# Kernel tuning notes

Hardware: AMD Instinct MI355X
Metric: run time of the kernel (lower is better)

Reference implementation:

```python
import jax, jax.numpy as jnp
import numpy as np

B, E, S, H, HD, M, MLP = 8, 1024, 2000, 16, 64, 10, 4096
EPS = 1e-5

def setup_inputs() -> dict:
    key = jax.random.key(0)
    ks = jax.random.split(key, 12)
    s = lambda k, shape, sc: jax.random.normal(k, shape, dtype=jnp.float32) * sc
    return {
        'X': s(ks[0], (B, E, S), 1.0),
        'Wq': s(ks[1], (H, HD, E), E ** -0.5), 'bq': s(ks[2], (H, HD), 0.02),
        'Wk': s(ks[3], (H, HD, E), E ** -0.5), 'bk': s(ks[4], (H, HD), 0.02),
        'Wv': s(ks[5], (H, HD, E), E ** -0.5), 'bv': s(ks[6], (H, HD), 0.02),
        'g1': jnp.ones((E,), jnp.float32), 'be1': jnp.zeros((E,), jnp.float32),
        'W1': s(ks[7], (MLP, E), E ** -0.5), 'b1': s(ks[8], (MLP,), 0.02),
        'W2': s(ks[9], (E, MLP), MLP ** -0.5), 'b2': s(ks[10], (E,), 0.02),
        'g2': jnp.ones((E,), jnp.float32), 'be2': jnp.zeros((E,), jnp.float32),
    }

def iterative_inv(K, n_iter=6):
    I = jnp.eye(K.shape[-1], dtype=K.dtype)
    # global (over all batch/head) max row-sum * max col-sum init, as in Nystromformer
    V = K.swapaxes(-1, -2) / (jnp.max(jnp.sum(jnp.abs(K), axis=-2)) * jnp.max(jnp.sum(jnp.abs(K), axis=-1)))
    for _ in range(n_iter):
        KV = K @ V
        V = 0.25 * V @ (13.0 * I - KV @ (15.0 * I - KV @ (7.0 * I - KV)))
    return V

def layer_norm(x, g, b):
    mu = jnp.mean(x, axis=-1, keepdims=True)
    var = jnp.var(x, axis=-1, keepdims=True)
    return (x - mu) * jax.lax.rsqrt(var + EPS) * g + b

def reference(X, Wq, bq, Wk, bk, Wv, bv, g1, be1, W1, b1, W2, b2, g2, be2):
    x = jnp.swapaxes(X, 1, 2)  # (B, S, E)
    # per-head projections (stacked): (B, H, S, HD)
    Q = jnp.einsum('bse,hde->bhsd', x, Wq) + bq[None, :, None, :]
    K = jnp.einsum('bse,hde->bhsd', x, Wk) + bk[None, :, None, :]
    V = jnp.einsum('bse,hde->bhsd', x, Wv) + bv[None, :, None, :]
    scale = 1.0 / np.sqrt(np.sqrt(HD)).astype(np.float32)
    Q = Q * scale
    K = K * scale
    # landmarks: mean over segments of length S//M -> (B, H, M, HD)
    Ql = Q.reshape(B, H, M, S // M, HD).mean(axis=-2)
    Kl = K.reshape(B, H, M, S // M, HD).mean(axis=-2)
    k1 = jax.nn.softmax(jnp.einsum('bhsd,bhmd->bhsm', Q, Kl), axis=-1)   # (B,H,S,M)
    k2 = jax.nn.softmax(jnp.einsum('bhnd,bhmd->bhnm', Ql, Kl), axis=-1)  # (B,H,M,M)
    k3 = jax.nn.softmax(jnp.einsum('bhmd,bhsd->bhms', Ql, K), axis=-1)   # (B,H,M,S)
    attn = (k1 @ iterative_inv(k2)) @ (k3 @ V)  # (B,H,S,HD)
    attn = jnp.swapaxes(attn, 1, 2).reshape(B, S, E)
    h = layer_norm(attn, g1, be1)
    h = jax.nn.gelu(h @ W1.T + b1, approximate=False)
    h = h @ W2.T + b2
    h = layer_norm(h, g2, be2)
    return jnp.swapaxes(h, 2, 1)  # (B, E, S)
```

## Files before the change

### kernel.cpp

```cpp
#include <hip/hip_runtime.h>
#include <cmath>
#include <cstdint>
#include <cstddef>

#define BB 8
#define EE 1024
#define SS 2000
#define HH 16
#define HDIM 64
#define MLM 10
#define MLPD 4096
#define QKV_N 3072
#define MPAD 16384
#define QK_SCALE 0.35355339059327373f

typedef __attribute__((ext_vector_type(8))) short short8v;
typedef __attribute__((ext_vector_type(4))) float f32x4;

static __device__ __forceinline__ short f2bf(float x) {
  unsigned u = __builtin_bit_cast(unsigned, x);
  unsigned r = (u + 0x7fffu + ((u >> 16) & 1u)) >> 16;
  return (short)(unsigned short)r;
}
static __device__ __forceinline__ float bf2f(short x) {
  unsigned u = ((unsigned)(unsigned short)x) << 16;
  return __builtin_bit_cast(float, u);
}

static __device__ __forceinline__ void load_lds16(const short* g, short* l) {
  __builtin_amdgcn_global_load_lds(
      (const __attribute__((address_space(1))) void*)g,
      (__attribute__((address_space(3))) void*)l, 16, 0, 0);
}

__global__ __launch_bounds__(256) void transpose_x(const float* __restrict__ X, short* __restrict__ xb) {
  __shared__ float tile[32][33];
  int b = blockIdx.z;
  int e0 = blockIdx.y * 32;
  int s0 = blockIdx.x * 32;
  int tx = threadIdx.x;
  int ty = threadIdx.y;
#pragma unroll
  for (int i = 0; i < 32; i += 8) {
    int e = e0 + ty + i, s = s0 + tx;
    tile[ty + i][tx] = (s < SS) ? X[((size_t)b * EE + e) * SS + s] : 0.f;
  }
  __syncthreads();
#pragma unroll
  for (int i = 0; i < 32; i += 8) {
    int s = s0 + ty + i, e = e0 + tx;
    if (s < SS) xb[((size_t)b * SS + s) * EE + e] = f2bf(tile[tx][ty + i]);
  }
}

__global__ __launch_bounds__(256) void cast_f2b(const float* __restrict__ src, short* __restrict__ dst, int n) {
  int i = blockIdx.x * 256 + threadIdx.x;
  int stride = gridDim.x * 256;
  for (; i < n; i += stride) dst[i] = f2bf(src[i]);
}

__global__ __launch_bounds__(512, 2) void gemm256(
    const short* __restrict__ A, const short* __restrict__ Bm, void* __restrict__ Cv,
    int K, int N, int mode, int Mstore,
    const float* __restrict__ p0, const float* __restrict__ p1, const float* __restrict__ p2)
{
  __shared__ __align__(16) short lds[65536];
  const int tid = threadIdx.x;

  const int xcd = blockIdx.x & 7;
  const int idx = blockIdx.x >> 3;
  const int m0 = (((xcd << 3) | (idx & 7))) << 8;
  const int n0 = (idx >> 3) << 8;

  const int lane = tid & 63, wv = tid >> 6;
  const int wm = wv >> 2, wn = wv & 3;
  const int lm = lane & 15, quad = lane >> 4;
  const int swz = ((lm >> 3) & 1) << 1;
  const int aoff = (wm * 128 + lm) * 32 + ((quad ^ swz) << 3);
  const int boff = (wn * 64  + lm) * 32 + ((quad ^ swz) << 3);

  const int srow = tid >> 2;
  const int ssl  = ((tid & 3) ^ (((tid >> 5) & 1) << 1)) << 3;
  const short* Ag = A + (size_t)(m0 + srow) * K + ssl;
  const short* Bg = Bm + (size_t)(n0 + srow) * K + ssl;
  const int wofs = wv << 9;

  f32x4 acc[8][4];
#pragma unroll
  for (int i = 0; i < 8; i++)
#pragma unroll
    for (int j = 0; j < 4; j++) acc[i][j] = (f32x4){0.f, 0.f, 0.f, 0.f};
  short8v afr[8], bfr[4];

#define RGN(buf, op, kh) (&lds[((((buf)*2 + (op)) * 2 + (kh)) << 13)])
#define STG(op, buf, kh, kt) do {                                          \
    const short* gp_ = ((op) ? Bg : Ag) + ((kt) * 64 + (kh) * 32);         \
    short* lp_ = RGN(buf, op, kh) + wofs;                                  \
    load_lds16(gp_, lp_);                                                  \
    load_lds16(gp_ + (size_t)128 * K, lp_ + 4096);                         \
  } while (0)
#define LDA(buf, kh) do {                                                  \
    const short* r_ = RGN(buf, 0, kh) + aoff;                              \
    _Pragma("unroll") for (int i_ = 0; i_ < 8; ++i_)                       \
      afr[i_] = *(const short8v*)(r_ + i_ * 512);                          \
  } while (0)
#define LDB(buf, kh, jb) do {                                              \
    const short* r_ = RGN(buf, 1, kh) + boff;                              \
    bfr[jb]     = *(const short8v*)(r_ + (jb) * 512);                      \
    bfr[(jb)+1] = *(const short8v*)(r_ + ((jb)+1) * 512);                  \
  } while (0)
#define MM(jb) do {                                                        \
    __builtin_amdgcn_s_setprio(1);                                         \
    _Pragma("unroll") for (int i_ = 0; i_ < 8; ++i_) {                     \
      acc[i_][jb]     = __builtin_amdgcn_mfma_f32_16x16x32_bf16(           \
          afr[i_], bfr[jb],     acc[i_][jb],     0, 0, 0);                 \
      acc[i_][(jb)+1] = __builtin_amdgcn_mfma_f32_16x16x32_bf16(           \
          afr[i_], bfr[(jb)+1], acc[i_][(jb)+1], 0, 0, 0);                 \
    }                                                                      \
    __builtin_amdgcn_s_setprio(0);                                         \
  } while (0)
#define SBAR() asm volatile("s_barrier" ::: "memory")
#define WAITV(n) asm volatile("s_waitcnt vmcnt(" #n ")" ::: "memory")

#define ITER(it, LAST) do {                                                              \
    LDB(0,0,0); LDA(0,0); STG(1,1,1, 2*(it)+1);                   SBAR(); MM(0); SBAR(); \
    LDB(0,0,2);           if (!(LAST)) STG(0,0,0, 2*(it)+2);      SBAR(); MM(2); SBAR(); \
    LDB(0,1,0); LDA(0,1); if (!(LAST)) STG(1,0,0, 2*(it)+2);      SBAR(); MM(0); SBAR(); \
    LDB(0,1,2);           if (!(LAST)) { STG(0,0,1, 2*(it)+2); WAITV(6); }               \
                          else         { WAITV(0); }              SBAR(); MM(2); SBAR(); \
    LDB(1,0,0); LDA(1,0); if (!(LAST)) STG(1,0,1, 2*(it)+2);      SBAR(); MM(0); SBAR(); \
    LDB(1,0,2);           if (!(LAST)) STG(0,1,0, 2*(it)+3);      SBAR(); MM(2); SBAR(); \
    LDB(1,1,0); LDA(1,1); if (!(LAST)) STG(1,1,0, 2*(it)+3);      SBAR(); MM(0); SBAR(); \
    LDB(1,1,2);           if (!(LAST)) { STG(0,1,1, 2*(it)+3); WAITV(6); }               \
                                                                  SBAR(); MM(2); SBAR(); \
  } while (0)

  const int NI = K >> 7;
  STG(0,0,0, 0); STG(1,0,0, 0); STG(0,0,1, 0); STG(1,0,1, 0);
  STG(0,1,0, 1); STG(1,1,0, 1); STG(0,1,1, 1);
  WAITV(6);
  SBAR();

  for (int it = 0; it < NI - 1; ++it) ITER(it, 0);
  ITER(NI - 1, 1);

  const int crow0 = m0 + wm * 128 + quad * 4;
  const int ccol0 = n0 + wn * 64 + lm;
#pragma unroll
  for (int j = 0; j < 4; ++j) {
    const int col = ccol0 + j * 16;
    float bias, scl = 1.f;
    if (mode == 0) {
      if (col < 1024)      { bias = p0[col];        scl = QK_SCALE; }
      else if (col < 2048) { bias = p1[col - 1024]; scl = QK_SCALE; }
      else                 { bias = p2[col - 2048]; }
    } else {
      bias = p0[col];
    }
#pragma unroll
    for (int i = 0; i < 8; ++i) {
#pragma unroll
      for (int r = 0; r < 4; ++r) {
        const int row = crow0 + i * 16 + r;
        if (row < Mstore) {
          float v = acc[i][j][r] + bias;
          if (mode == 0)      v *= scl;
          else if (mode == 1) v = 0.5f * v * (1.f + erff(v * 0.70710678118f));
          if (mode == 2) ((float*)Cv)[(size_t)row * N + col] = v;
          else           ((short*)Cv)[(size_t)row * N + col] = f2bf(v);
        }
      }
    }
  }
#undef RGN
#undef STG
#undef LDA
#undef LDB
#undef MM
#undef SBAR
#undef WAITV
#undef ITER
}

__global__ __launch_bounds__(64) void landmarks(const short* __restrict__ QKV, float* __restrict__ Ql, float* __restrict__ Kl) {
  int d = threadIdx.x;
  int bhm = blockIdx.x;
  int part = blockIdx.y;
  int b = bhm / (HH * MLM);
  int h = (bhm / MLM) % HH;
  int m = bhm % MLM;
  const short* src = QKV + (part ? 1024 : 0);
  size_t base = ((size_t)(b * SS + m * 200)) * QKV_N + h * HDIM + d;
  float acc = 0.f;
  for (int i = 0; i < 200; i++) acc += bf2f(src[base + (size_t)i * QKV_N]);
  float* dst = part ? Kl : Ql;
  dst[((size_t)(b * HH + h) * MLM + m) * HDIM + d] = acc * (1.f / 200.f);
}

__global__ __launch_bounds__(128) void k2stats(const float* __restrict__ Ql, const float* __restrict__ Kl,
                                               float* __restrict__ k2, float* __restrict__ cmax, float* __restrict__ rmax) {
  int bh = blockIdx.x;
  __shared__ float QlS[640], KlS[640], zz[100], k2s[100], cs[10], rs[10];
  for (int i = threadIdx.x; i < 640; i += 128) {
    QlS[i] = Ql[(size_t)bh * 640 + i];
    KlS[i] = Kl[(size_t)bh * 640 + i];
  }
  __syncthreads();
  if (threadIdx.x < 100) {
    int i = threadIdx.x / 10, j = threadIdx.x % 10;
    float z = 0.f;
    for (int d = 0; d < 64; d++) z += QlS[i * 64 + d] * KlS[j * 64 + d];
    zz[threadIdx.x] = z;
  }
  __syncthreads();
  if (threadIdx.x < 10) {
    int i = threadIdx.x;
    float mx = -1e30f;
    for (int j = 0; j < 10; j++) mx = fmaxf(mx, zz[i * 10 + j]);
    float s = 0.f, e[10];
    for (int j = 0; j < 10; j++) { e[j] = expf(zz[i * 10 + j] - mx); s += e[j]; }
    float inv = 1.f / s, rsum = 0.f;
    for (int j = 0; j < 10; j++) {
      float v = e[j] * inv;
      k2s[i * 10 + j] = v;
      k2[(size_t)bh * 100 + i * 10 + j] = v;
      rsum += v;
    }
    rs[i] = rsum;
  }
  __syncthreads();
  if (threadIdx.x < 10) {
    int j = threadIdx.x;
    float c = 0.f;
    for (int i = 0; i < 10; i++) c += k2s[i * 10 + j];
    cs[j] = c;
  }
  __syncthreads();
  if (threadIdx.x == 0) {
    float m1 = 0.f, m2 = 0.f;
    for (int j = 0; j < 10; j++) { m1 = fmaxf(m1, cs[j]); m2 = fmaxf(m2, rs[j]); }
    cmax[bh] = m1;
    rmax[bh] = m2;
  }
}

__global__ __launch_bounds__(128) void invk(const float* __restrict__ k2, const float* __restrict__ cmax,
                                            const float* __restrict__ rmax, float* __restrict__ invo) {
  int bh = blockIdx.x;
  __shared__ float gsc;
  __shared__ float Km[100], Vm[100], KV[100], Ta[100], Tb[100];
  if (threadIdx.x == 0) {
    float mc = 0.f, mr = 0.f;
    for (int i = 0; i < 128; i++) { mc = fmaxf(mc, cmax[i]); mr = fmaxf(mr, rmax[i]); }
    gsc = 1.f / (mc * mr);
  }
  for (int i = threadIdx.x; i < 100; i += 128) Km[i] = k2[(size_t)bh * 100 + i];
  __syncthreads();
  int t = threadIdx.x;
  int i = t / 10, j = t % 10;
  bool act = t < 100;
  if (act) Vm[t] = Km[j * 10 + i] * gsc;
  __syncthreads();
  for (int it = 0; it < 6; it++) {
    if (act) { float a = 0.f; for (int k = 0; k < 10; k++) a += Km[i * 10 + k] * Vm[k * 10 + j]; KV[t] = a; }
    __syncthreads();
    if (act) Ta[t] = (i == j ? 7.f : 0.f) - KV[t];
    __syncthreads();
    if (act) { float a = 0.f; for (int k = 0; k < 10; k++) a += KV[i * 10 + k] * Ta[k * 10 + j]; Tb[t] = (i == j ? 15.f : 0.f) - a; }
    __syncthreads();
    if (act) { float a = 0.f; for (int k = 0; k < 10; k++) a += KV[i * 10 + k] * Tb[k * 10 + j]; Ta[t] = (i == j ? 13.f : 0.f) - a; }
    __syncthreads();
    if (act) { float a = 0.f; for (int k = 0; k < 10; k++) a += Vm[i * 10 + k] * Ta[k * 10 + j]; Tb[t] = 0.25f * a; }
    __syncthreads();
    if (act) Vm[t] = Tb[t];
    __syncthreads();
  }
  if (act) invo[(size_t)bh * 100 + t] = Vm[t];
}

__global__ __launch_bounds__(256) void k1inv_kernel(const short* __restrict__ QKV, const float* __restrict__ Kl,
                                                    const float* __restrict__ invg, float* __restrict__ k1inv) {
  int b = blockIdx.y;
  int s0 = blockIdx.x * 16;
  __shared__ float KlS[16 * 650];
  __shared__ float invS[16 * 101];
  for (int idx = threadIdx.x; idx < 16 * 640; idx += 256) {
    int h = idx / 640, r = idx % 640;
    KlS[h * 650 + r] = Kl[(size_t)(b * HH + h) * 640 + r];
  }
  for (int idx = threadIdx.x; idx < 1600; idx += 256) {
    int h = idx / 100, r = idx % 100;
    invS[h * 101 + r] = invg[(size_t)(b * HH + h) * 100 + r];
  }
  __syncthreads();
  int sl = threadIdx.x >> 4, h = threadIdx.x & 15;
  int s = s0 + sl;
  size_t qoff = (size_t)(b * SS + s) * QKV_N + h * HDIM;
  float z[10];
#pragma unroll
  for (int m = 0; m < 10; m++) z[m] = 0.f;
  for (int c = 0; c < 8; c++) {
    short8v qv = *(const short8v*)&QKV[qoff + c * 8];
    float qf[8];
#pragma unroll
    for (int jj = 0; jj < 8; jj++) qf[jj] = bf2f(qv[jj]);
#pragma unroll
    for (int m = 0; m < 10; m++) {
      const float* kl = &KlS[h * 650 + m * 64 + c * 8];
      float a = 0.f;
#pragma unroll
      for (int jj = 0; jj < 8; jj++) a += qf[jj] * kl[jj];
      z[m] += a;
    }
  }
  float mx = z[0];
#pragma unroll
  for (int m = 1; m < 10; m++) mx = fmaxf(mx, z[m]);
  float p[10], ssum = 0.f;
#pragma unroll
  for (int m = 0; m < 10; m++) { p[m] = expf(z[m] - mx); ssum += p[m]; }
  float rinv = 1.f / ssum;
  float* dst = &k1inv[((size_t)(b * SS + s) * HH + h) * MLM];
#pragma unroll
  for (int mm = 0; mm < 10; mm++) {
    float a = 0.f;
#pragma unroll
    for (int jjj = 0; jjj < 10; jjj++) a += p[jjj] * invS[h * 101 + jjj * 10 + mm];
    dst[mm] = a * rinv;
  }
}

__global__ __launch_bounds__(256) void k3v_kernel(const short* __restrict__ QKV, const float* __restrict__ Qlg,
                                                  float* __restrict__ kvout) {
  int bh = blockIdx.x;
  int b = bh >> 4, h = bh & 15;
  __shared__ float Kt[64 * 65];
  __shared__ float Vt[64 * 65];
  __shared__ float eS[10 * 64];
  __shared__ float QlS[640];
  __shared__ float denS[10];
  int tid = threadIdx.x;
  int wave = tid >> 6, lane = tid & 63;
  for (int i = tid; i < 640; i += 256) QlS[i] = Qlg[(size_t)bh * 640 + i];
  float myden = 0.f;
  float accn[3] = {0.f, 0.f, 0.f};
  int rowi = tid >> 2;
  int d0 = (tid & 3) * 16;
  for (int s0 = 0; s0 < SS; s0 += 64) {
    __syncthreads();
    if (s0 + rowi < SS) {
      size_t base = (size_t)(b * SS + s0 + rowi) * QKV_N + h * HDIM + d0;
      short8v k0v = *(const short8v*)&QKV[base + 1024];
      short8v k1v = *(const short8v*)&QKV[base + 1024 + 8];
      short8v v0v = *(const short8v*)&QKV[base + 2048];
      short8v v1v = *(const short8v*)&QKV[base + 2048 + 8];
#pragma unroll
      for (int jj = 0; jj < 8; jj++) {
        Kt[rowi * 65 + d0 + jj]     = bf2f(k0v[jj]);
        Kt[rowi * 65 + d0 + 8 + jj] = bf2f(k1v[jj]);
        Vt[rowi * 65 + d0 + jj]     = bf2f(v0v[jj]);
        Vt[rowi * 65 + d0 + 8 + jj] = bf2f(v1v[jj]);
      }
    }
    __syncthreads();
    for (int mb = 0; mb < 12; mb += 4) {
      int m = mb + wave;
      if (m < 10) {
        float z = 0.f;
        const float* kr = &Kt[lane * 65];
        const float* ql = &QlS[m * 64];
        for (int d = 0; d < 64; d++) z += ql[d] * kr[d];
        eS[m * 64 + lane] = (s0 + lane < SS) ? expf(z) : 0.f;
      }
    }
    __syncthreads();
    if (tid < 10) {
      float a = 0.f;
      for (int slj = 0; slj < 64; slj++) a += eS[tid * 64 + slj];
      myden += a;
    }
#pragma unroll
    for (int ii = 0; ii < 3; ii++) {
      int idx = tid + ii * 256;
      if (idx < 640) {
        int m = idx >> 6, d = idx & 63;
        float a = 0.f;
        for (int slj = 0; slj < 64; slj++) a += eS[m * 64 + slj] * Vt[slj * 65 + d];
        accn[ii] += a;
      }
    }
  }
  if (tid < 10) denS[tid] = myden;
  __syncthreads();
#pragma unroll
  for (int ii = 0; ii < 3; ii++) {
    int idx = tid + ii * 256;
    if (idx < 640) {
      int m = idx >> 6;
      kvout[(size_t)bh * 640 + idx] = accn[ii] / denS[m];
    }
  }
}

__global__ __launch_bounds__(256) void attn_ln1(const float* __restrict__ k1inv, const float* __restrict__ kvg,
                                                const float* __restrict__ g1, const float* __restrict__ be1,
                                                short* __restrict__ h1) {
  int blk = blockIdx.x;
  int b = blk / SS;
  __shared__ float pS[160];
  __shared__ float red[8];
  for (int i = threadIdx.x; i < 160; i += 256) pS[i] = k1inv[(size_t)blk * 160 + i];
  __syncthreads();
  float vals[4], s1 = 0.f, s2 = 0.f;
#pragma unroll
  for (int i = 0; i < 4; i++) {
    int e = threadIdx.x + i * 256;
    int h = e >> 6, d = e & 63;
    const float* kvp = &kvg[((size_t)(b * HH + h) * MLM) * HDIM + d];
    const float* pp = &pS[h * 10];
    float a = 0.f;
#pragma unroll
    for (int m = 0; m < 10; m++) a += pp[m] * kvp[m * 64];
    vals[i] = a; s1 += a; s2 += a * a;
  }
#pragma unroll
  for (int off = 32; off; off >>= 1) { s1 += __shfl_down(s1, off); s2 += __shfl_down(s2, off); }
  int wv = threadIdx.x >> 6;
  if ((threadIdx.x & 63) == 0) { red[wv] = s1; red[4 + wv] = s2; }
  __syncthreads();
  float t1 = red[0] + red[1] + red[2] + red[3];
  float t2 = red[4] + red[5] + red[6] + red[7];
  float mean = t1 * (1.f / 1024.f);
  float var = t2 * (1.f / 1024.f) - mean * mean;
  float ninv = rsqrtf(var + 1e-5f);
#pragma unroll
  for (int i = 0; i < 4; i++) {
    int e = threadIdx.x + i * 256;
    h1[(size_t)blk * EE + e] = f2bf((vals[i] - mean) * ninv * g1[e] + be1[e]);
  }
}

__global__ __launch_bounds__(256) void ln2_kernel(const float* __restrict__ h2, const float* __restrict__ g2,
                                                  const float* __restrict__ be2, short* __restrict__ h3) {
  int blk = blockIdx.x;
  __shared__ float red[8];
  float vals[4], s1 = 0.f, s2 = 0.f;
#pragma unroll
  for (int i = 0; i < 4; i++) {
    int e = threadIdx.x + i * 256;
    float a = h2[(size_t)blk * EE + e];
    vals[i] = a; s1 += a; s2 += a * a;
  }
#pragma unroll
  for (int off = 32; off; off >>= 1) { s1 += __shfl_down(s1, off); s2 += __shfl_down(s2, off); }
  int wv = threadIdx.x >> 6;
  if ((threadIdx.x & 63) == 0) { red[wv] = s1; red[4 + wv] = s2; }
  __syncthreads();
  float t1 = red[0] + red[1] + red[2] + red[3];
  float t2 = red[4] + red[5] + red[6] + red[7];
  float mean = t1 * (1.f / 1024.f);
  float var = t2 * (1.f / 1024.f) - mean * mean;
  float ninv = rsqrtf(var + 1e-5f);
#pragma unroll
  for (int i = 0; i < 4; i++) {
    int e = threadIdx.x + i * 256;
    h3[(size_t)blk * EE + e] = f2bf((vals[i] - mean) * ninv * g2[e] + be2[e]);
  }
}

__global__ __launch_bounds__(256) void transpose_out(const short* __restrict__ h3, float* __restrict__ outp) {
  __shared__ short tile[64 * 65];
  int b = blockIdx.z;
  int e0 = blockIdx.y * 64;
  int s0 = blockIdx.x * 64;
  int tx = threadIdx.x & 63;
  int ty = threadIdx.x >> 6;
#pragma unroll
  for (int i = 0; i < 16; i++) {
    int r = ty + i * 4;
    int s = s0 + r;
    if (s < SS) tile[r * 65 + tx] = h3[((size_t)b * SS + s) * EE + e0 + tx];
  }
  __syncthreads();
#pragma unroll
  for (int i = 0; i < 16; i++) {
    int c = ty + i * 4;
    int s = s0 + tx;
    if (s < SS) outp[((size_t)b * EE + e0 + c) * SS + s] = bf2f(tile[tx * 65 + c]);
  }
}

#define ALIGN_UP(x) (((x) + 255) & ~(size_t)255)
static const size_t SZ_SLOTA = (size_t)MPAD * EE * 2;
static const size_t SZ_QKV   = (size_t)MPAD * QKV_N * 2;
static const size_t SZ_MID   = (size_t)MPAD * MLPD * 2;
static const size_t SZ_WCAT  = (size_t)QKV_N * EE * 2;
static const size_t SZ_W1B   = (size_t)MLPD * EE * 2;
static const size_t SZ_W2B   = (size_t)EE * MLPD * 2;
static const size_t SZ_QL    = (size_t)BB * HH * MLM * HDIM * 4;
static const size_t SZ_K2    = (size_t)BB * HH * 100 * 4;
static const size_t SZ_ST    = 512;

extern "C" void kernel_launch(void* const* d_in, const int* in_sizes, int n_in,
                              void* d_out, int out_size, void* d_ws, size_t ws_size,
                              hipStream_t stream) {
  const float* X   = (const float*)d_in[0];
  const float* Wq  = (const float*)d_in[1];
  const float* bq  = (const float*)d_in[2];
  const float* Wk  = (const float*)d_in[3];
  const float* bk  = (const float*)d_in[4];
  const float* Wv  = (const float*)d_in[5];
  const float* bv  = (const float*)d_in[6];
  const float* g1  = (const float*)d_in[7];
  const float* be1 = (const float*)d_in[8];
  const float* W1  = (const float*)d_in[9];
  const float* b1  = (const float*)d_in[10];
  const float* W2  = (const float*)d_in[11];
  const float* b2  = (const float*)d_in[12];
  const float* g2  = (const float*)d_in[13];
  const float* be2 = (const float*)d_in[14];

  char* ws = (char*)d_ws;
  size_t off = 0;
  char* slotA = ws + off; off += ALIGN_UP(SZ_SLOTA);
  char* slotB = ws + off; off += ALIGN_UP(SZ_MID);
  char* slotD = ws + off; off += ALIGN_UP(SZ_WCAT);
  short* W1b = (short*)(ws + off); off += ALIGN_UP(SZ_W1B);
  short* W2b = (short*)(ws + off); off += ALIGN_UP(SZ_W2B);

  short* xb   = (short*)slotA;
  short* h1   = (short*)slotA;
  short* h3   = (short*)slotA;
  short* qkv  = (short*)slotB;
  short* mid  = (short*)slotB;
  float* k1ib = (float*)(slotB + ALIGN_UP(SZ_QKV));
  short* Wcat = (short*)slotD;
  size_t doff = 0;
  float* Qlm  = (float*)(slotD + doff); doff += ALIGN_UP(SZ_QL);
  float* Klm  = (float*)(slotD + doff); doff += ALIGN_UP(SZ_QL);
  float* k2b  = (float*)(slotD + doff); doff += ALIGN_UP(SZ_K2);
  float* cmaxb= (float*)(slotD + doff); doff += ALIGN_UP(SZ_ST);
  float* rmaxb= (float*)(slotD + doff); doff += ALIGN_UP(SZ_ST);
  float* invb = (float*)(slotD + doff); doff += ALIGN_UP(SZ_K2);
  float* kvb  = (float*)(slotD + doff); doff += ALIGN_UP(SZ_QL);
  float* h2c  = (float*)d_out;
  (void)ws_size; (void)in_sizes; (void)n_in; (void)out_size;

  hipMemsetAsync(slotA + (size_t)BB * SS * EE * 2, 0,
                 (size_t)(MPAD - BB * SS) * EE * 2, stream);
  transpose_x<<<dim3(63, 32, BB), dim3(32, 8), 0, stream>>>(X, xb);
  cast_f2b<<<2048, 256, 0, stream>>>(Wq, Wcat,             EE * EE);
  cast_f2b<<<2048, 256, 0, stream>>>(Wk, Wcat + EE * EE,   EE * EE);
  cast_f2b<<<2048, 256, 0, stream>>>(Wv, Wcat + 2*EE*EE,   EE * EE);
  cast_f2b<<<4096, 256, 0, stream>>>(W1, W1b, MLPD * EE);
  cast_f2b<<<4096, 256, 0, stream>>>(W2, W2b, EE * MLPD);
  gemm256<<<64 * 12, 512, 0, stream>>>(xb, Wcat, qkv, EE, QKV_N, 0, MPAD, bq, bk, bv);
  landmarks<<<dim3(BB * HH * MLM, 2), 64, 0, stream>>>(qkv, Qlm, Klm);
  k2stats<<<BB * HH, 128, 0, stream>>>(Qlm, Klm, k2b, cmaxb, rmaxb);
  invk<<<BB * HH, 128, 0, stream>>>(k2b, cmaxb, rmaxb, invb);
  k1inv_kernel<<<dim3(125, BB), 256, 0, stream>>>(qkv, Klm, invb, k1ib);
  k3v_kernel<<<BB * HH, 256, 0, stream>>>(qkv, Qlm, kvb);
  attn_ln1<<<BB * SS, 256, 0, stream>>>(k1ib, kvb, g1, be1, h1);
  gemm256<<<64 * 16, 512, 0, stream>>>(h1, W1b, mid, EE, MLPD, 1, MPAD, b1, nullptr, nullptr);
  gemm256<<<64 * 4, 512, 0, stream>>>(mid, W2b, h2c, MLPD, EE, 2, BB * SS, b2, nullptr, nullptr);
  ln2_kernel<<<BB * SS, 256, 0, stream>>>(h2c, g2, be2, h3);
  transpose_out<<<dim3(32, 16, BB), 256, 0, stream>>>(h3, (float*)d_out);
}
```

Baseline: 983.1 us.

## Double-buffer GEMM register fragments and approximate GELU erf with polynomial

Rewrites the bf16 MFMA GEMM main loop to hold two register fragment sets, so LDS reads for the next k-half are issued while MFMAs run on the current one. It also cuts the per-k-step barrier count and stages whole 64-wide k tiles at once. Separately, it replaces erff in the GELU epilogue with the Abramowitz-Stegun polynomial plus __expf to make the MLP epilogue cheaper. The costs are higher register pressure from the duplicated fragments and a small approximation error in GELU (about 1e-7 absolute in erf).

```diff
diff --git a/kernel.cpp b/kernel.cpp
--- a/kernel.cpp
+++ b/kernel.cpp
@@ -27,6 +27,18 @@
   return __builtin_bit_cast(float, u);
 }
 
+static __device__ __forceinline__ float gelu_f(float v) {
+  float x = v * 0.70710678118f;
+  float ax = fabsf(x);
+  float t = 1.f / (1.f + 0.3275911f * ax);
+  float poly = t * (0.254829592f + t * (-0.284496736f + t * (1.421413741f +
+               t * (-1.453152027f + t * 1.061405429f))));
+  float e = __expf(-ax * ax);
+  float erf_ax = 1.f - poly * e;
+  float er = (x < 0.f) ? -erf_ax : erf_ax;
+  return 0.5f * v * (1.f + er);
+}
+
 static __device__ __forceinline__ void load_lds16(const short* g, short* l) {
   __builtin_amdgcn_global_load_lds(
       (const __attribute__((address_space(1))) void*)g,
@@ -90,7 +102,7 @@
   for (int i = 0; i < 8; i++)
 #pragma unroll
     for (int j = 0; j < 4; j++) acc[i][j] = (f32x4){0.f, 0.f, 0.f, 0.f};
-  short8v afr[8], bfr[4];
+  short8v afr0[8], bfr0[4], afr1[8], bfr1[4];
 
 #define RGN(buf, op, kh) (&lds[((((buf)*2 + (op)) * 2 + (kh)) << 13)])
 #define STG(op, buf, kh, kt) do {                                          \
@@ -99,50 +111,53 @@
     load_lds16(gp_, lp_);                                                  \
     load_lds16(gp_ + (size_t)128 * K, lp_ + 4096);                         \
   } while (0)
-#define LDA(buf, kh) do {                                                  \
-    const short* r_ = RGN(buf, 0, kh) + aoff;                              \
+#define STGALL(buf, kt) do {                                               \
+    STG(0, buf, 0, kt); STG(1, buf, 0, kt);                                \
+    STG(0, buf, 1, kt); STG(1, buf, 1, kt);                                \
+  } while (0)
+#define LDSET(S, buf, kh) do {                                             \
+    const short* ra_ = RGN(buf, 0, kh) + aoff;                             \
+    const short* rb_ = RGN(buf, 1, kh) + boff;                             \
     _Pragma("unroll") for (int i_ = 0; i_ < 8; ++i_)                       \
-      afr[i_] = *(const short8v*)(r_ + i_ * 512);                          \
+      afr##S[i_] = *(const short8v*)(ra_ + i_ * 512);                      \
+    _Pragma("unroll") for (int j_ = 0; j_ < 4; ++j_)                       \
+      bfr##S[j_] = *(const short8v*)(rb_ + j_ * 512);                      \
   } while (0)
-#define LDB(buf, kh, jb) do {                                              \
-    const short* r_ = RGN(buf, 1, kh) + boff;                              \
-    bfr[jb]     = *(const short8v*)(r_ + (jb) * 512);                      \
-    bfr[(jb)+1] = *(const short8v*)(r_ + ((jb)+1) * 512);                  \
-  } while (0)
-#define MM(jb) do {                                                        \
+#define MMS(S) do {                                                        \
     __builtin_amdgcn_s_setprio(1);                                         \
-    _Pragma("unroll") for (int i_ = 0; i_ < 8; ++i_) {                     \
-      acc[i_][jb]     = __builtin_amdgcn_mfma_f32_16x16x32_bf16(           \
-          afr[i_], bfr[jb],     acc[i_][jb],     0, 0, 0);                 \
-      acc[i_][(jb)+1] = __builtin_amdgcn_mfma_f32_16x16x32_bf16(           \
-          afr[i_], bfr[(jb)+1], acc[i_][(jb)+1], 0, 0, 0);                 \
-    }                                                                      \
+    _Pragma("unroll") for (int i_ = 0; i_ < 8; ++i_)                       \
+      _Pragma("unroll") for (int j_ = 0; j_ < 4; ++j_)                     \
+        acc[i_][j_] = __builtin_amdgcn_mfma_f32_16x16x32_bf16(             \
+            afr##S[i_], bfr##S[j_], acc[i_][j_], 0, 0, 0);                 \
     __builtin_amdgcn_s_setprio(0);                                         \
   } while (0)
 #define SBAR() asm volatile("s_barrier" ::: "memory")
 #define WAITV(n) asm volatile("s_waitcnt vmcnt(" #n ")" ::: "memory")
-
-#define ITER(it, LAST) do {                                                              \
-    LDB(0,0,0); LDA(0,0); STG(1,1,1, 2*(it)+1);                   SBAR(); MM(0); SBAR(); \
-    LDB(0,0,2);           if (!(LAST)) STG(0,0,0, 2*(it)+2);      SBAR(); MM(2); SBAR(); \
-    LDB(0,1,0); LDA(0,1); if (!(LAST)) STG(1,0,0, 2*(it)+2);      SBAR(); MM(0); SBAR(); \
-    LDB(0,1,2);           if (!(LAST)) { STG(0,0,1, 2*(it)+2); WAITV(6); }               \
-                          else         { WAITV(0); }              SBAR(); MM(2); SBAR(); \
-    LDB(1,0,0); LDA(1,0); if (!(LAST)) STG(1,0,1, 2*(it)+2);      SBAR(); MM(0); SBAR(); \
-    LDB(1,0,2);           if (!(LAST)) STG(0,1,0, 2*(it)+3);      SBAR(); MM(2); SBAR(); \
-    LDB(1,1,0); LDA(1,1); if (!(LAST)) STG(1,1,0, 2*(it)+3);      SBAR(); MM(0); SBAR(); \
-    LDB(1,1,2);           if (!(LAST)) { STG(0,1,1, 2*(it)+3); WAITV(6); }               \
-                                                                  SBAR(); MM(2); SBAR(); \
+#define WAITL(n) asm volatile("s_waitcnt lgkmcnt(" #n ")" ::: "memory")
+
+#define KTILE(buf, tt, t2, NT) do {                                        \
+    LDSET(1, buf, 1);                      \
+    MMS(0);                                                                \
+    WAITL(0);                        \
+    SBAR();                                             \
+    if ((t2) < (NT)) STGALL(buf, t2);    \
+    MMS(1);                                \
+    if ((t2) < (NT)) { WAITV(8); } else { WAITV(0); }                      \
+    SBAR();                            \
   } while (0)
 
-  const int NI = K >> 7;
-  STG(0,0,0, 0); STG(1,0,0, 0); STG(0,0,1, 0); STG(1,0,1, 0);
-  STG(0,1,0, 1); STG(1,1,0, 1); STG(0,1,1, 1);
-  WAITV(6);
+  const int NT = K >> 6;
+  STGALL(0, 0); STGALL(1, 1);
+  WAITV(8);
   SBAR();
-
-  for (int it = 0; it < NI - 1; ++it) ITER(it, 0);
-  ITER(NI - 1, 1);
+  LDSET(0, 0, 0);
+
+  for (int t = 0; t < NT; t += 2) {
+    KTILE(0, t, t + 2, NT);
+    LDSET(0, 1, 0);
+    KTILE(1, t + 1, t + 3, NT);
+    if (t + 2 < NT) LDSET(0, 0, 0);
+  }
 
   const int crow0 = m0 + wm * 128 + quad * 4;
   const int ccol0 = n0 + wn * 64 + lm;
@@ -165,7 +180,7 @@
         if (row < Mstore) {
           float v = acc[i][j][r] + bias;
           if (mode == 0)      v *= scl;
-          else if (mode == 1) v = 0.5f * v * (1.f + erff(v * 0.70710678118f));
+          else if (mode == 1) v = gelu_f(v);
           if (mode == 2) ((float*)Cv)[(size_t)row * N + col] = v;
           else           ((short*)Cv)[(size_t)row * N + col] = f2bf(v);
         }
@@ -174,12 +189,13 @@
   }
 #undef RGN
 #undef STG
-#undef LDA
-#undef LDB
-#undef MM
+#undef STGALL
+#undef LDSET
+#undef MMS
 #undef SBAR
 #undef WAITV
-#undef ITER
+#undef WAITL
+#undef KTILE
 }
 
 __global__ __launch_bounds__(64) void landmarks(const short* __restrict__ QKV, float* __restrict__ Ql, float* __restrict__ Kl) {
```

Measured after the change: 1.155 ms. 1.17x slower.
